# Optimization experiments

Measured on AMD Instinct MI355X. Metric: run time of the kernel, lower is better.

The kernel has to match this reference:

```python
import jax, jax.numpy as jnp
import numpy as np

SEGMENT_LENGTHS = [1024, 2048, 4096]
DILATION_RATES = [1, 2, 4]


def _head_groups(num_heads, num_segments):
    base = num_heads // num_segments
    extra = num_heads % num_segments
    groups = [base] * num_segments
    for i in range(extra):
        groups[-(i + 1)] += 1
    return groups


def _dilated_indices(segment_len, dilation_rate, offset):
    # Mirrors RingDilatedAttentionV2._apply_dilation index construction (static).
    if dilation_rate > 1:
        idx = np.arange(offset, segment_len, dilation_rate)
        repeats = (segment_len + len(idx) - 1) // len(idx)
        idx = np.tile(idx, repeats)[:segment_len] % segment_len
    else:
        idx = np.arange(segment_len)
    return jnp.asarray(idx, dtype=jnp.int32)


def setup_inputs() -> dict:
    key = jax.random.key(0)
    kq, kk, kv = jax.random.split(key, 3)
    b, n, h, d = 1, 4096, 12, 64
    return {
        "query": jax.random.normal(kq, (b, n, h, d), dtype=jnp.float32),
        "key": jax.random.normal(kk, (b, n, h, d), dtype=jnp.float32),
        "value": jax.random.normal(kv, (b, n, h, d), dtype=jnp.float32),
        "is_causal": 1,
    }


def _dilated_attention(query, key, value, is_causal):
    b, n, h, d = query.shape
    groups = _head_groups(h, len(SEGMENT_LENGTHS))
    scale = 1.0 / np.sqrt(d).astype(np.float32)
    outs = []
    head_start = 0
    for i, (seg_len, rate, g) in enumerate(zip(SEGMENT_LENGTHS, DILATION_RATES, groups)):
        if g == 0:
            continue
        sl = min(seg_len, n)
        ns = n // sl  # n chosen divisible by every segment length
        q = query[:, :, head_start:head_start + g, :].reshape(b, ns, sl, g, d)
        k = key[:, :, head_start:head_start + g, :].reshape(b, ns, sl, g, d)
        v = value[:, :, head_start:head_start + g, :].reshape(b, ns, sl, g, d)
        if rate > 1 or i > 0:
            idx = _dilated_indices(sl, rate, i)
            k = k[:, :, idx]
            v = v[:, :, idx]
        # scores: [b, seg, heads, q_pos, k_pos]
        scores = jnp.einsum("bsqhd,bskhd->bshqk", q, k) * scale
        if is_causal:
            causal = jnp.triu(jnp.ones((sl, sl), dtype=bool), k=1)
            scores = jnp.where(causal, jnp.finfo(scores.dtype).min, scores)
        attn = jax.nn.softmax(scores, axis=-1)
        o = jnp.einsum("bshqk,bskhd->bsqhd", attn, v).reshape(b, n, g, d)
        outs.append(o)
        head_start += g
    return jnp.concatenate(outs, axis=2)  # [b, n, h, d]


def reference(query, key, value, is_causal):
    return _dilated_attention(query, key, value, is_causal)
```

## Files before the change

kernel.cpp:

```cpp
#include <hip/hip_runtime.h>
#include <hip/hip_bf16.h>
#include <math.h>

typedef __bf16 bf16x8 __attribute__((ext_vector_type(8)));
typedef float  f32x4  __attribute__((ext_vector_type(4)));
typedef unsigned short ushort_t;

#define LDK 72

#define KG_OFF  0
#define VGT_OFF 6291456
#define LACC_OFF 12582912

__device__ __forceinline__ int gather_pos(int gi, int group) {
    const int lsl = 10 + group;
    const int seg = gi >> lsl;
    const int j   = gi - (seg << lsl);
    return (seg << lsl) + group + ((j & 1023) << group);
}

__device__ __forceinline__ void gld_lds16(const ushort_t* g, __bf16* l) {
    __builtin_amdgcn_global_load_lds(
        (const __attribute__((address_space(1))) void*)g,
        (__attribute__((address_space(3))) void*)l, 16, 0, 0);
}

__global__ __launch_bounds__(256)
void preconvert_kernel(const float* __restrict__ K, const float* __restrict__ V,
                       ushort_t* __restrict__ Kg, ushort_t* __restrict__ VgT)
{
    const int HD = 768;
    int b = blockIdx.x;
    const int tid = threadIdx.x;
    if (b < 768) {
        const int h = b % 12, gi0 = (b / 12) * 64;
        const int group = h >> 2;
        const int gi = gi0 + (tid >> 2);
        const int d0 = (tid & 3) << 4;
        const int pos = gather_pos(gi, group);
        const float* kp = K + (size_t)pos * HD + h * 64 + d0;
        float4 x0 = ((const float4*)kp)[0], x1 = ((const float4*)kp)[1];
        float4 x2 = ((const float4*)kp)[2], x3 = ((const float4*)kp)[3];
        bf16x8 w0, w1;
        w0[0]=(__bf16)x0.x; w0[1]=(__bf16)x0.y; w0[2]=(__bf16)x0.z; w0[3]=(__bf16)x0.w;
        w0[4]=(__bf16)x1.x; w0[5]=(__bf16)x1.y; w0[6]=(__bf16)x1.z; w0[7]=(__bf16)x1.w;
        w1[0]=(__bf16)x2.x; w1[1]=(__bf16)x2.y; w1[2]=(__bf16)x2.z; w1[3]=(__bf16)x2.w;
        w1[4]=(__bf16)x3.x; w1[5]=(__bf16)x3.y; w1[6]=(__bf16)x3.z; w1[7]=(__bf16)x3.w;
        ushort_t* out = Kg + ((size_t)(h * 4096 + gi)) * 64 + d0;
        *(bf16x8*)out = w0;
        *(bf16x8*)(out + 8) = w1;
    } else {
        b -= 768;
        const int h = b % 12, gi0 = (b / 12) * 64;
        const int group = h >> 2;
        __shared__ __align__(16) __bf16 Ts[64 * LDK];
        const int gil = tid >> 2;
        const int d0 = (tid & 3) << 4;
        const int pos = gather_pos(gi0 + gil, group);
        const float* vp = V + (size_t)pos * HD + h * 64 + d0;
        float4 x0 = ((const float4*)vp)[0], x1 = ((const float4*)vp)[1];
        float4 x2 = ((const float4*)vp)[2], x3 = ((const float4*)vp)[3];
        bf16x8 w0, w1;
        w0[0]=(__bf16)x0.x; w0[1]=(__bf16)x0.y; w0[2]=(__bf16)x0.z; w0[3]=(__bf16)x0.w;
        w0[4]=(__bf16)x1.x; w0[5]=(__bf16)x1.y; w0[6]=(__bf16)x1.z; w0[7]=(__bf16)x1.w;
        w1[0]=(__bf16)x2.x; w1[1]=(__bf16)x2.y; w1[2]=(__bf16)x2.z; w1[3]=(__bf16)x2.w;
        w1[4]=(__bf16)x3.x; w1[5]=(__bf16)x3.y; w1[6]=(__bf16)x3.z; w1[7]=(__bf16)x3.w;
        *(bf16x8*)&Ts[gil * LDK + d0]     = w0;
        *(bf16x8*)&Ts[gil * LDK + d0 + 8] = w1;
        __syncthreads();
        const int d = tid >> 2, c = tid & 3;
        bf16x8 o0, o1;
        #pragma unroll
        for (int i = 0; i < 8; ++i) {
            o0[i] = Ts[(c * 16 + i) * LDK + d];
            o1[i] = Ts[(c * 16 + 8 + i) * LDK + d];
        }
        ushort_t* out = VgT + ((size_t)(h * 64 + d)) * 4096 + gi0 + c * 16;
        *(bf16x8*)out = o0;
        *(bf16x8*)(out + 8) = o1;
    }
}

__global__ __launch_bounds__(256)
void dilated_attn_kernel(const float* __restrict__ Q,
                         const ushort_t* __restrict__ Kg,
                         const ushort_t* __restrict__ VgT,
                         const int* __restrict__ is_causal_p,
                         float* __restrict__ Out,
                         float* __restrict__ l_acc)
{
    const int HD = 768;
    const int bx  = blockIdx.x;
    const int qt  = 63 - (bx / 48);
    const int rem = bx % 48;
    const int h   = rem % 12;
    const int c   = rem / 12;
    const int group = h >> 2;
    const int sl    = 1024 << group;
    const int causal = (*is_causal_p) != 0;

    const int q0 = qt << 6;
    const int qb = q0 & (sl - 1);
    const int seg_start = q0 - qb;
    const int diag_kt = qb >> 6;
    const int nkt = causal ? (diag_kt + 1) : (sl >> 6);
    const int kt0 = c << 4;
    if (kt0 >= nkt) return;
    const int kend = min(kt0 + 16, nkt);
    const int nch  = (nkt + 15) >> 4;

    const int tid  = threadIdx.x;
    const int wave = tid >> 6;
    const int lane = tid & 63;
    const int l15  = lane & 15;
    const int quad = lane >> 4;

    __shared__ __align__(16) __bf16 Ks[2][64 * 64];
    __shared__ __align__(16) __bf16 Vs[2][64 * 64];
    __shared__ __align__(16) __bf16 Ps[4][16 * 64];

    const ushort_t* kg_head = Kg + (size_t)h * 4096 * 64;
    const ushort_t* vt_head = VgT + (size_t)h * 64 * 4096;

    const int bx16  = ((lane & 7) ^ (lane >> 3)) << 3;
    const int krow0 = wave * 16 + (lane >> 3);
    const int koff0 = krow0 * 64 + bx16;
    const int koff1 = koff0 + 8 * 64;
    const size_t voff0 = (size_t)krow0 * 4096 + bx16;
    const size_t voff1 = voff0 + (size_t)8 * 4096;

    auto stage = [&](int kt, int buf) {
        const ushort_t* kb = kg_head + ((size_t)(seg_start + (kt << 6)) << 6);
        const ushort_t* vb = vt_head + seg_start + (kt << 6);
        __bf16* kl = &Ks[buf][wave * 1024];
        __bf16* vl = &Vs[buf][wave * 1024];
        gld_lds16(kb + koff0, kl);
        gld_lds16(kb + koff1, kl + 512);
        gld_lds16(vb + voff0, vl);
        gld_lds16(vb + voff1, vl + 512);
    };

    const int qrow = q0 + wave * 16 + l15;
    const float* qptr = Q + (size_t)qrow * HD + h * 64;
    bf16x8 a0, a1;
    {
        const float s = 0.125f * 1.4426950408889634f;
        float4 x0 = ((const float4*)(qptr + quad * 8))[0];
        float4 x1 = ((const float4*)(qptr + quad * 8))[1];
        float4 y0 = ((const float4*)(qptr + 32 + quad * 8))[0];
        float4 y1 = ((const float4*)(qptr + 32 + quad * 8))[1];
        a0[0]=(__bf16)(x0.x*s); a0[1]=(__bf16)(x0.y*s); a0[2]=(__bf16)(x0.z*s); a0[3]=(__bf16)(x0.w*s);
        a0[4]=(__bf16)(x1.x*s); a0[5]=(__bf16)(x1.y*s); a0[6]=(__bf16)(x1.z*s); a0[7]=(__bf16)(x1.w*s);
        a1[0]=(__bf16)(y0.x*s); a1[1]=(__bf16)(y0.y*s); a1[2]=(__bf16)(y0.z*s); a1[3]=(__bf16)(y0.w*s);
        a1[4]=(__bf16)(y1.x*s); a1[5]=(__bf16)(y1.y*s); a1[6]=(__bf16)(y1.z*s); a1[7]=(__bf16)(y1.w*s);
    }

    f32x4 o[4];
    #pragma unroll
    for (int t = 0; t < 4; ++t) o[t] = (f32x4){0.f, 0.f, 0.f, 0.f};
    float l_r[4] = {0.f, 0.f, 0.f, 0.f};

    stage(kt0, 0);
    __syncthreads();

    for (int kt = kt0; kt < kend; ++kt) {
        const int cur = (kt - kt0) & 1;
        if (kt + 1 < kend) stage(kt + 1, cur ^ 1);

        f32x4 sacc[4];
        __builtin_amdgcn_s_setprio(1);
        #pragma unroll
        for (int t = 0; t < 4; ++t) {
            const int krow = t * 16 + l15;
            const int xk = (krow & 7) << 3;
            bf16x8 b0 = *(const bf16x8*)&Ks[cur][krow * 64 + ((quad << 3) ^ xk)];
            bf16x8 b1 = *(const bf16x8*)&Ks[cur][krow * 64 + (((quad + 4) << 3) ^ xk)];
            f32x4 cc = (f32x4){0.f, 0.f, 0.f, 0.f};
            cc = __builtin_amdgcn_mfma_f32_16x16x32_bf16(a0, b0, cc, 0, 0, 0);
            cc = __builtin_amdgcn_mfma_f32_16x16x32_bf16(a1, b1, cc, 0, 0, 0);
            sacc[t] = cc;
        }
        __builtin_amdgcn_s_setprio(0);

        const bool isdiag = causal && (kt == diag_kt);
        #pragma unroll
        for (int t = 0; t < 4; ++t) {
            const int col = t * 16 + l15;
            const int cb  = t * 2 + (l15 >> 3);
            #pragma unroll
            for (int r = 0; r < 4; ++r) {
                const int prow = quad * 4 + r;
                const int row = wave * 16 + prow;
                float p = exp2f(sacc[t][r]);
                if (isdiag && col > row) p = 0.f;
                l_r[r] += p;
                Ps[wave][prow * 64 + ((cb ^ (prow & 7)) << 3) + (l15 & 7)] = (__bf16)p;
            }
        }

        const int xp = (l15 & 7) << 3;
        bf16x8 p0 = *(const bf16x8*)&Ps[wave][l15 * 64 + ((quad << 3) ^ xp)];
        bf16x8 p1 = *(const bf16x8*)&Ps[wave][l15 * 64 + (((quad + 4) << 3) ^ xp)];
        __builtin_amdgcn_s_setprio(1);
        #pragma unroll
        for (int t = 0; t < 4; ++t) {
            const int vrow = t * 16 + l15;
            const int xv = (vrow & 7) << 3;
            bf16x8 bv0 = *(const bf16x8*)&Vs[cur][vrow * 64 + ((quad << 3) ^ xv)];
            bf16x8 bv1 = *(const bf16x8*)&Vs[cur][vrow * 64 + (((quad + 4) << 3) ^ xv)];
            o[t] = __builtin_amdgcn_mfma_f32_16x16x32_bf16(p0, bv0, o[t], 0, 0, 0);
            o[t] = __builtin_amdgcn_mfma_f32_16x16x32_bf16(p1, bv1, o[t], 0, 0, 0);
        }
        __builtin_amdgcn_s_setprio(0);

        __syncthreads();
    }

    #pragma unroll
    for (int off = 1; off < 16; off <<= 1) {
        #pragma unroll
        for (int r = 0; r < 4; ++r)
            l_r[r] += __shfl_xor(l_r[r], off, 64);
    }
    if (nch == 1) {
        #pragma unroll
        for (int r = 0; r < 4; ++r) {
            const float inv = 1.0f / l_r[r];
            const int row = q0 + wave * 16 + quad * 4 + r;
            #pragma unroll
            for (int t = 0; t < 4; ++t)
                Out[(size_t)row * HD + h * 64 + t * 16 + l15] = o[t][r] * inv;
        }
    } else {
        #pragma unroll
        for (int r = 0; r < 4; ++r) {
            const int row = q0 + wave * 16 + quad * 4 + r;
            if (l15 == 0) atomicAdd(&l_acc[row * 12 + h], l_r[r]);
            #pragma unroll
            for (int t = 0; t < 4; ++t)
                atomicAdd(&Out[(size_t)row * HD + h * 64 + t * 16 + l15], o[t][r]);
        }
    }
}

__global__ __launch_bounds__(256)
void finalize_kernel(float* __restrict__ Out, const float* __restrict__ l_acc,
                     const int* __restrict__ is_causal_p)
{
    const int causal = (*is_causal_p) != 0;
    const int idx = blockIdx.x * 256 + threadIdx.x;
    const int rh = idx >> 4;
    const int d4 = idx & 15;
    const int h = rh % 12;
    const int row = rh / 12;
    const int group = h >> 2;
    const int ntf = 16 << group;
    const int qt = row >> 6;
    const int nkt = causal ? ((qt & (ntf - 1)) + 1) : ntf;
    if (nkt <= 16) return;
    const float inv = 1.0f / l_acc[rh];
    float4* p = (float4*)Out + (size_t)rh * 16 + d4;
    float4 v = *p;
    v.x *= inv; v.y *= inv; v.z *= inv; v.w *= inv;
    *p = v;
}

extern "C" void kernel_launch(void* const* d_in, const int* in_sizes, int n_in,
                              void* d_out, int out_size, void* d_ws, size_t ws_size,
                              hipStream_t stream) {
    (void)in_sizes; (void)n_in; (void)out_size; (void)ws_size;
    const float* Q = (const float*)d_in[0];
    const float* K = (const float*)d_in[1];
    const float* V = (const float*)d_in[2];
    const int* isc = (const int*)d_in[3];
    float* Out = (float*)d_out;
    ushort_t* Kg   = (ushort_t*)((char*)d_ws + KG_OFF);
    ushort_t* VgT  = (ushort_t*)((char*)d_ws + VGT_OFF);
    float*    lacc = (float*)((char*)d_ws + LACC_OFF);

    hipMemsetAsync(Out, 0, (size_t)4096 * 12 * 64 * 4, stream);
    hipMemsetAsync(lacc, 0, (size_t)4096 * 12 * 4, stream);
    preconvert_kernel<<<1536, 256, 0, stream>>>(K, V, Kg, VgT);
    dilated_attn_kernel<<<3072, 256, 0, stream>>>(Q, Kg, VgT, isc, Out, lacc);
    finalize_kernel<<<3072, 256, 0, stream>>>(Out, lacc, isc);
}
```

Measured before the change: 155.3 us.

## Use 32x32x16 MFMA with 128-row query tiles and register-resident P

Switches the attention kernel from 16x16x32 MFMA on 64-row query tiles to 32x32x16 MFMA on 128-row tiles, with each wave owning 32 query rows. Scores are computed transposed (K as A operand), so P can be repacked into the PV operand with lane shuffles instead of a round trip through shared memory. Each K/V tile loaded now serves twice as many query rows, and waves skip tiles past their own diagonal. In exchange the grid is halved, which reduces parallelism. The causal diagonal handling now spans two key tiles per block, and finalize's chunk-count logic is updated to match.

```diff
diff --git a/kernel.cpp b/kernel.cpp
--- a/kernel.cpp
+++ b/kernel.cpp
@@ -4,6 +4,8 @@
 
 typedef __bf16 bf16x8 __attribute__((ext_vector_type(8)));
 typedef float  f32x4  __attribute__((ext_vector_type(4)));
+typedef float  f32x16 __attribute__((ext_vector_type(16)));
+typedef unsigned int uint4v __attribute__((ext_vector_type(4)));
 typedef unsigned short ushort_t;
 
 #define LDK 72
@@ -23,6 +25,19 @@
     __builtin_amdgcn_global_load_lds(
         (const __attribute__((address_space(1))) void*)g,
         (__attribute__((address_space(3))) void*)l, 16, 0, 0);
+}
+
+__device__ __forceinline__ unsigned int pk_bf16(float lo, float hi) {
+    unsigned short a = __builtin_bit_cast(unsigned short, (__bf16)lo);
+    unsigned short b = __builtin_bit_cast(unsigned short, (__bf16)hi);
+    return ((unsigned int)b << 16) | (unsigned int)a;
+}
+
+__device__ __forceinline__ f32x16 zero16() {
+    f32x16 z;
+    #pragma unroll
+    for (int i = 0; i < 16; ++i) z[i] = 0.f;
+    return z;
 }
 
 __global__ __launch_bounds__(256)
@@ -91,7 +106,7 @@
 {
     const int HD = 768;
     const int bx  = blockIdx.x;
-    const int qt  = 63 - (bx / 48);
+    const int qt  = 31 - (bx / 48);
     const int rem = bx % 48;
     const int h   = rem % 12;
     const int c   = rem / 12;
@@ -99,11 +114,11 @@
     const int sl    = 1024 << group;
     const int causal = (*is_causal_p) != 0;
 
-    const int q0 = qt << 6;
+    const int q0 = qt << 7;
     const int qb = q0 & (sl - 1);
     const int seg_start = q0 - qb;
-    const int diag_kt = qb >> 6;
-    const int nkt = causal ? (diag_kt + 1) : (sl >> 6);
+    const int blk_diag = (qb + 127) >> 6;
+    const int nkt = causal ? (blk_diag + 1) : (sl >> 6);
     const int kt0 = c << 4;
     if (kt0 >= nkt) return;
     const int kend = min(kt0 + 16, nkt);
@@ -112,53 +127,50 @@
     const int tid  = threadIdx.x;
     const int wave = tid >> 6;
     const int lane = tid & 63;
-    const int l15  = lane & 15;
-    const int quad = lane >> 4;
+    const int l31  = lane & 31;
+    const int hi   = lane >> 5;
 
     __shared__ __align__(16) __bf16 Ks[2][64 * 64];
     __shared__ __align__(16) __bf16 Vs[2][64 * 64];
-    __shared__ __align__(16) __bf16 Ps[4][16 * 64];
 
     const ushort_t* kg_head = Kg + (size_t)h * 4096 * 64;
     const ushort_t* vt_head = VgT + (size_t)h * 64 * 4096;
 
-    const int bx16  = ((lane & 7) ^ (lane >> 3)) << 3;
-    const int krow0 = wave * 16 + (lane >> 3);
-    const int koff0 = krow0 * 64 + bx16;
-    const int koff1 = koff0 + 8 * 64;
-    const size_t voff0 = (size_t)krow0 * 4096 + bx16;
-    const size_t voff1 = voff0 + (size_t)8 * 4096;
+    const int bx16 = (((lane & 7) ^ (lane >> 3)) & 7) << 3;
+    const int r8   = lane >> 3;
 
     auto stage = [&](int kt, int buf) {
         const ushort_t* kb = kg_head + ((size_t)(seg_start + (kt << 6)) << 6);
         const ushort_t* vb = vt_head + seg_start + (kt << 6);
-        __bf16* kl = &Ks[buf][wave * 1024];
-        __bf16* vl = &Vs[buf][wave * 1024];
-        gld_lds16(kb + koff0, kl);
-        gld_lds16(kb + koff1, kl + 512);
-        gld_lds16(vb + voff0, vl);
-        gld_lds16(vb + voff1, vl + 512);
+        #pragma unroll
+        for (int i = 0; i < 2; ++i) {
+            const int row = i * 32 + wave * 8 + r8;
+            gld_lds16(kb + row * 64 + bx16, &Ks[buf][(i * 32 + wave * 8) * 64]);
+            gld_lds16(vb + (size_t)row * 4096 + bx16, &Vs[buf][(i * 32 + wave * 8) * 64]);
+        }
     };
 
-    const int qrow = q0 + wave * 16 + l15;
+    const int qrow = q0 + wave * 32 + l31;
     const float* qptr = Q + (size_t)qrow * HD + h * 64;
-    bf16x8 a0, a1;
+    bf16x8 qf[4];
     {
         const float s = 0.125f * 1.4426950408889634f;
-        float4 x0 = ((const float4*)(qptr + quad * 8))[0];
-        float4 x1 = ((const float4*)(qptr + quad * 8))[1];
-        float4 y0 = ((const float4*)(qptr + 32 + quad * 8))[0];
-        float4 y1 = ((const float4*)(qptr + 32 + quad * 8))[1];
-        a0[0]=(__bf16)(x0.x*s); a0[1]=(__bf16)(x0.y*s); a0[2]=(__bf16)(x0.z*s); a0[3]=(__bf16)(x0.w*s);
-        a0[4]=(__bf16)(x1.x*s); a0[5]=(__bf16)(x1.y*s); a0[6]=(__bf16)(x1.z*s); a0[7]=(__bf16)(x1.w*s);
-        a1[0]=(__bf16)(y0.x*s); a1[1]=(__bf16)(y0.y*s); a1[2]=(__bf16)(y0.z*s); a1[3]=(__bf16)(y0.w*s);
-        a1[4]=(__bf16)(y1.x*s); a1[5]=(__bf16)(y1.y*s); a1[6]=(__bf16)(y1.z*s); a1[7]=(__bf16)(y1.w*s);
+        #pragma unroll
+        for (int ds = 0; ds < 4; ++ds) {
+            float4 x0 = ((const float4*)(qptr + ds * 16 + hi * 8))[0];
+            float4 x1 = ((const float4*)(qptr + ds * 16 + hi * 8))[1];
+            bf16x8 w;
+            w[0]=(__bf16)(x0.x*s); w[1]=(__bf16)(x0.y*s); w[2]=(__bf16)(x0.z*s); w[3]=(__bf16)(x0.w*s);
+            w[4]=(__bf16)(x1.x*s); w[5]=(__bf16)(x1.y*s); w[6]=(__bf16)(x1.z*s); w[7]=(__bf16)(x1.w*s);
+            qf[ds] = w;
+        }
     }
 
-    f32x4 o[4];
-    #pragma unroll
-    for (int t = 0; t < 4; ++t) o[t] = (f32x4){0.f, 0.f, 0.f, 0.f};
-    float l_r[4] = {0.f, 0.f, 0.f, 0.f};
+    const int mydiag = causal ? ((qb + wave * 32 + 31) >> 6) : 0x7fffffff;
+    const int lrow   = ((wave & 1) << 5) + l31;
+
+    f32x16 o0 = zero16(), o1 = zero16();
+    float l_part = 0.f;
 
     stage(kt0, 0);
     __syncthreads();
@@ -167,78 +179,88 @@
         const int cur = (kt - kt0) & 1;
         if (kt + 1 < kend) stage(kt + 1, cur ^ 1);
 
-        f32x4 sacc[4];
-        __builtin_amdgcn_s_setprio(1);
-        #pragma unroll
-        for (int t = 0; t < 4; ++t) {
-            const int krow = t * 16 + l15;
-            const int xk = (krow & 7) << 3;
-            bf16x8 b0 = *(const bf16x8*)&Ks[cur][krow * 64 + ((quad << 3) ^ xk)];
-            bf16x8 b1 = *(const bf16x8*)&Ks[cur][krow * 64 + (((quad + 4) << 3) ^ xk)];
-            f32x4 cc = (f32x4){0.f, 0.f, 0.f, 0.f};
-            cc = __builtin_amdgcn_mfma_f32_16x16x32_bf16(a0, b0, cc, 0, 0, 0);
-            cc = __builtin_amdgcn_mfma_f32_16x16x32_bf16(a1, b1, cc, 0, 0, 0);
-            sacc[t] = cc;
-        }
-        __builtin_amdgcn_s_setprio(0);
-
-        const bool isdiag = causal && (kt == diag_kt);
-        #pragma unroll
-        for (int t = 0; t < 4; ++t) {
-            const int col = t * 16 + l15;
-            const int cb  = t * 2 + (l15 >> 3);
+        if (kt <= mydiag) {
+            f32x16 s0 = zero16(), s1 = zero16();
+            const int xr = (l31 & 7);
+            __builtin_amdgcn_s_setprio(1);
             #pragma unroll
-            for (int r = 0; r < 4; ++r) {
-                const int prow = quad * 4 + r;
-                const int row = wave * 16 + prow;
-                float p = exp2f(sacc[t][r]);
-                if (isdiag && col > row) p = 0.f;
-                l_r[r] += p;
-                Ps[wave][prow * 64 + ((cb ^ (prow & 7)) << 3) + (l15 & 7)] = (__bf16)p;
+            for (int ds = 0; ds < 4; ++ds) {
+                const int cb = ds * 2 + hi;
+                bf16x8 k0 = *(const bf16x8*)&Ks[cur][l31 * 64        + ((cb ^ xr) << 3)];
+                bf16x8 k1 = *(const bf16x8*)&Ks[cur][(32 + l31) * 64 + ((cb ^ xr) << 3)];
+                s0 = __builtin_amdgcn_mfma_f32_32x32x16_bf16(k0, qf[ds], s0, 0, 0, 0);
+                s1 = __builtin_amdgcn_mfma_f32_32x32x16_bf16(k1, qf[ds], s1, 0, 0, 0);
             }
-        }
-
-        const int xp = (l15 & 7) << 3;
-        bf16x8 p0 = *(const bf16x8*)&Ps[wave][l15 * 64 + ((quad << 3) ^ xp)];
-        bf16x8 p1 = *(const bf16x8*)&Ps[wave][l15 * 64 + (((quad + 4) << 3) ^ xp)];
-        __builtin_amdgcn_s_setprio(1);
-        #pragma unroll
-        for (int t = 0; t < 4; ++t) {
-            const int vrow = t * 16 + l15;
-            const int xv = (vrow & 7) << 3;
-            bf16x8 bv0 = *(const bf16x8*)&Vs[cur][vrow * 64 + ((quad << 3) ^ xv)];
-            bf16x8 bv1 = *(const bf16x8*)&Vs[cur][vrow * 64 + (((quad + 4) << 3) ^ xv)];
-            o[t] = __builtin_amdgcn_mfma_f32_16x16x32_bf16(p0, bv0, o[t], 0, 0, 0);
-            o[t] = __builtin_amdgcn_mfma_f32_16x16x32_bf16(p1, bv1, o[t], 0, 0, 0);
-        }
-        __builtin_amdgcn_s_setprio(0);
+            __builtin_amdgcn_s_setprio(0);
+
+            float p[2][16];
+            const bool isdiag = causal && (kt == mydiag);
+            #pragma unroll
+            for (int r = 0; r < 16; ++r) {
+                float v0 = exp2f(s0[r]);
+                float v1 = exp2f(s1[r]);
+                if (isdiag) {
+                    const int kl = (r & 3) + ((r >> 2) << 3) + (hi << 2);
+                    if (kl > lrow)      v0 = 0.f;
+                    if (kl + 32 > lrow) v1 = 0.f;
+                }
+                p[0][r] = v0; p[1][r] = v1;
+                l_part += v0 + v1;
+            }
+
+            __builtin_amdgcn_s_setprio(1);
+            #pragma unroll
+            for (int b = 0; b < 2; ++b) {
+                #pragma unroll
+                for (int ks2 = 0; ks2 < 2; ++ks2) {
+                    const int g = ks2 * 8;
+                    unsigned int x0 = pk_bf16(p[b][g + 0], p[b][g + 1]);
+                    unsigned int x1 = pk_bf16(p[b][g + 2], p[b][g + 3]);
+                    unsigned int y0 = pk_bf16(p[b][g + 4], p[b][g + 5]);
+                    unsigned int y1 = pk_bf16(p[b][g + 6], p[b][g + 7]);
+                    unsigned int sx0 = (unsigned int)__shfl_xor((int)x0, 32);
+                    unsigned int sx1 = (unsigned int)__shfl_xor((int)x1, 32);
+                    unsigned int sy0 = (unsigned int)__shfl_xor((int)y0, 32);
+                    unsigned int sy1 = (unsigned int)__shfl_xor((int)y1, 32);
+                    uint4v t;
+                    t[0] = hi ? sy0 : x0;
+                    t[1] = hi ? sy1 : x1;
+                    t[2] = hi ? y0 : sx0;
+                    t[3] = hi ? y1 : sx1;
+                    bf16x8 pa = __builtin_bit_cast(bf16x8, t);
+                    const int kcb = (b * 2 + ks2) * 2 + hi;
+                    bf16x8 v0 = *(const bf16x8*)&Vs[cur][l31 * 64        + ((kcb ^ xr) << 3)];
+                    bf16x8 v1 = *(const bf16x8*)&Vs[cur][(32 + l31) * 64 + ((kcb ^ xr) << 3)];
+                    o0 = __builtin_amdgcn_mfma_f32_32x32x16_bf16(pa, v0, o0, 0, 0, 0);
+                    o1 = __builtin_amdgcn_mfma_f32_32x32x16_bf16(pa, v1, o1, 0, 0, 0);
+                }
+            }
+            __builtin_amdgcn_s_setprio(0);
+        }
 
         __syncthreads();
     }
 
-    #pragma unroll
-    for (int off = 1; off < 16; off <<= 1) {
-        #pragma unroll
-        for (int r = 0; r < 4; ++r)
-            l_r[r] += __shfl_xor(l_r[r], off, 64);
-    }
+    const float l2 = l_part + __shfl_xor(l_part, 32);
+    const int qw = q0 + wave * 32;
     if (nch == 1) {
-        #pragma unroll
-        for (int r = 0; r < 4; ++r) {
-            const float inv = 1.0f / l_r[r];
-            const int row = q0 + wave * 16 + quad * 4 + r;
-            #pragma unroll
-            for (int t = 0; t < 4; ++t)
-                Out[(size_t)row * HD + h * 64 + t * 16 + l15] = o[t][r] * inv;
+        const float inv = 1.0f / l2;
+        #pragma unroll
+        for (int r = 0; r < 16; ++r) {
+            const int qloc = (r & 3) + ((r >> 2) << 3) + (hi << 2);
+            const float invq = __shfl(inv, qloc);
+            const int row = qw + qloc;
+            Out[(size_t)row * HD + h * 64 + l31]      = o0[r] * invq;
+            Out[(size_t)row * HD + h * 64 + 32 + l31] = o1[r] * invq;
         }
     } else {
-        #pragma unroll
-        for (int r = 0; r < 4; ++r) {
-            const int row = q0 + wave * 16 + quad * 4 + r;
-            if (l15 == 0) atomicAdd(&l_acc[row * 12 + h], l_r[r]);
-            #pragma unroll
-            for (int t = 0; t < 4; ++t)
-                atomicAdd(&Out[(size_t)row * HD + h * 64 + t * 16 + l15], o[t][r]);
+        if (hi == 0) atomicAdd(&l_acc[(qw + l31) * 12 + h], l2);
+        #pragma unroll
+        for (int r = 0; r < 16; ++r) {
+            const int qloc = (r & 3) + ((r >> 2) << 3) + (hi << 2);
+            const int row = qw + qloc;
+            atomicAdd(&Out[(size_t)row * HD + h * 64 + l31],      o0[r]);
+            atomicAdd(&Out[(size_t)row * HD + h * 64 + 32 + l31], o1[r]);
         }
     }
 }
@@ -255,8 +277,9 @@
     const int row = rh / 12;
     const int group = h >> 2;
     const int ntf = 16 << group;
-    const int qt = row >> 6;
-    const int nkt = causal ? ((qt & (ntf - 1)) + 1) : ntf;
+    const int qt128 = row >> 7;
+    const int qb_t = (qt128 << 1) & (ntf - 1);
+    const int nkt = causal ? (qb_t + 2) : ntf;
     if (nkt <= 16) return;
     const float inv = 1.0f / l_acc[rh];
     float4* p = (float4*)Out + (size_t)rh * 16 + d4;
@@ -281,6 +304,6 @@
     hipMemsetAsync(Out, 0, (size_t)4096 * 12 * 64 * 4, stream);
     hipMemsetAsync(lacc, 0, (size_t)4096 * 12 * 4, stream);
     preconvert_kernel<<<1536, 256, 0, stream>>>(K, V, Kg, VgT);
-    dilated_attn_kernel<<<3072, 256, 0, stream>>>(Q, Kg, VgT, isc, Out, lacc);
+    dilated_attn_kernel<<<1536, 256, 0, stream>>>(Q, Kg, VgT, isc, Out, lacc);
     finalize_kernel<<<3072, 256, 0, stream>>>(Out, lacc, isc);
 }
```

Result: faster. 148.7 us (-4.3%).
